# Performance work log

Measured on AMD Instinct MI355X. Metric: run time of the kernel, lower is better.

The kernel has to match this reference:

```python
import jax, jax.numpy as jnp
import numpy as np
from jax import lax

B, P, W, C = 32, 256, 16, 64
H = 128          # hidden_dim
PRED = 64        # pred_stat_len
TOK = W + 1      # token_len
SIGMA_MIN = 1e-3
EPS = 1e-5


def setup_inputs() -> dict:
    key = jax.random.key(0)
    ks = jax.random.split(key, 20)
    s = 0.05
    inp = {
        "mu_hist": jax.random.normal(ks[0], (B, P, C), jnp.float32),
        "std_hist": jax.random.uniform(ks[1], (B, P, C), jnp.float32, 0.1, 1.5),
        "anchor": jax.random.normal(ks[2], (B, 1, C), jnp.float32),
        "raw_patches": jax.random.normal(ks[3], (B, P, W, C), jnp.float32),
        # mean branch params
        "mean_in_W": jax.random.normal(ks[4], (TOK, H), jnp.float32) * s,
        "mean_in_b": jax.random.normal(ks[5], (H,), jnp.float32) * s,
        "mean_a_logit": jnp.full((H,), float(np.log(9.0)), jnp.float32),
        "mean_post_W": jax.random.normal(ks[6], (H, H), jnp.float32) * s,
        "mean_post_b": jax.random.normal(ks[7], (H,), jnp.float32) * s,
        "mean_out_W": jax.random.normal(ks[8], (H, PRED), jnp.float32) * s,
        "mean_out_b": jax.random.normal(ks[9], (PRED,), jnp.float32) * s,
        "gamma_mu": jax.random.normal(ks[10], (C,), jnp.float32) * s,
        # std branch params
        "std_in_W": jax.random.normal(ks[11], (TOK, H), jnp.float32) * s,
        "std_in_b": jax.random.normal(ks[12], (H,), jnp.float32) * s,
        "std_a_logit": jnp.full((H,), float(np.log(9.0)), jnp.float32),
        "std_post_W": jax.random.normal(ks[13], (H, H), jnp.float32) * s,
        "std_post_b": jax.random.normal(ks[14], (H,), jnp.float32) * s,
        "std_out_W": jax.random.normal(ks[15], (H, PRED), jnp.float32) * s,
        "std_out_b": jax.random.normal(ks[16], (PRED,), jnp.float32) * s,
        "gamma_std": jax.random.normal(ks[17], (C,), jnp.float32) * s,
    }
    return inp


def _ema(u, a_logit):
    # u: (BC, P, H) -> final hidden state (BC, H) via h_t = a*h + (1-a)*u_t
    a = jax.nn.sigmoid(a_logit)
    one_minus_a = 1.0 - a

    def step(h, u_t):
        return a * h + one_minus_a * u_t, None

    h0 = jnp.zeros((u.shape[0], u.shape[2]), u.dtype)
    h, _ = lax.scan(step, h0, jnp.swapaxes(u, 0, 1))  # scan over P
    return h


def _branch(token, in_W, in_b, a_logit, post_W, post_b, out_W, out_b):
    u = token @ in_W + in_b                     # (BC, P, H)
    h = _ema(u, a_logit)                        # (BC, H)
    h = h + jax.nn.gelu(h, approximate=False) @ post_W + post_b
    res = h @ out_W + out_b                     # (BC, PRED)
    return res.reshape(B, C, PRED).transpose(0, 2, 1)  # (B, PRED, C)


def reference(mu_hist, std_hist, anchor, raw_patches,
              mean_in_W, mean_in_b, mean_a_logit, mean_post_W, mean_post_b,
              mean_out_W, mean_out_b, gamma_mu,
              std_in_W, std_in_b, std_a_logit, std_post_W, std_post_b,
              std_out_W, std_out_b, gamma_std):
    BC = B * C
    # --- mean branch ---
    mu_center = mu_hist - anchor                                 # (B,P,C)
    raw_center = raw_patches - anchor[:, :, None, :]             # (B,P,W,C)
    mu_center_t = mu_center.transpose(0, 2, 1).reshape(BC, P, 1)
    raw_center_t = raw_center.transpose(0, 3, 1, 2).reshape(BC, P, W)
    mean_token = jnp.concatenate([mu_center_t, raw_center_t], axis=-1)
    mu_res = _branch(mean_token, mean_in_W, mean_in_b, mean_a_logit,
                     mean_post_W, mean_post_b, mean_out_W, mean_out_b)
    mu_fut = anchor + gamma_mu[None, None, :] * mu_res           # (B,PRED,C)

    # --- std branch ---
    logstd_hist = jnp.log(jnp.maximum(std_hist, SIGMA_MIN))      # (B,P,C)
    logstd_anchor = logstd_hist.mean(axis=1, keepdims=True)      # (B,1,C)
    logstd_center = logstd_hist - logstd_anchor
    z_patch = (raw_patches - mu_hist[:, :, None, :]) / (std_hist[:, :, None, :] + EPS)
    logstd_center_t = logstd_center.transpose(0, 2, 1).reshape(BC, P, 1)
    z_patch_t = z_patch.transpose(0, 3, 1, 2).reshape(BC, P, W)
    std_token = jnp.concatenate([logstd_center_t, z_patch_t], axis=-1)
    logstd_res = _branch(std_token, std_in_W, std_in_b, std_a_logit,
                         std_post_W, std_post_b, std_out_W, std_out_b)
    logstd_fut = logstd_anchor + gamma_std[None, None, :] * logstd_res
    std_fut = jnp.maximum(jnp.exp(logstd_fut), SIGMA_MIN)
    return mu_fut, std_fut
```

## Files before the change

kernel.cpp:

```cpp
#include <hip/hip_runtime.h>
#include <math.h>

#define Bn 32
#define Pn 256
#define Wn 16
#define Cn 64
#define Hn 128
#define PREDn 64
#define TOKn 17

__global__ void lsa_kernel(const float* __restrict__ std_hist,
                           float* __restrict__ lsa) {
  int b = blockIdx.x;
  int c = threadIdx.x & 63;
  int q = threadIdx.x >> 6;
  const float* base = std_hist + ((size_t)b * Pn) * Cn + c;
  float s = 0.f;
#pragma unroll
  for (int i = 0; i < 64; ++i) {
    int t = q + 4 * i;
    s += logf(fmaxf(base[(size_t)t * Cn], 1e-3f));
  }
  __shared__ float red[4][64];
  red[q][c] = s;
  __syncthreads();
  if (q == 0) {
    lsa[b * 64 + c] =
        (red[0][c] + red[1][c] + red[2][c] + red[3][c]) * (1.0f / 256.0f);
  }
}

__launch_bounds__(256, 2)
__global__ void ema_kernel(
    const float* __restrict__ mu_hist, const float* __restrict__ std_hist,
    const float* __restrict__ anchor, const float* __restrict__ raw,
    const float* __restrict__ mW, const float* __restrict__ mb, const float* __restrict__ mal,
    const float* __restrict__ sW, const float* __restrict__ sb, const float* __restrict__ sal,
    const float* __restrict__ lsa, float* __restrict__ Spart) {
  const int sx = blockIdx.x;
  const int cblk = sx & 1, hblk = (sx >> 1) & 1, ph = (sx >> 2) & 1;
  const int b = blockIdx.y, br = blockIdx.z;
  const int tid = threadIdx.x;
  const int cr = tid & 31;
  const int hhg = tid >> 5;

  const float* inW = br ? sW : mW;
  const float* inb = br ? sb : mb;
  const float* alog = br ? sal : mal;
  const int hh0 = hblk * 64 + hhg * 8;

  float Wr[TOKn][8];
#pragma unroll
  for (int k = 0; k < TOKn; ++k) {
    float4 w0 = *(const float4*)&inW[k * Hn + hh0];
    float4 w1 = *(const float4*)&inW[k * Hn + hh0 + 4];
    Wr[k][0] = w0.x; Wr[k][1] = w0.y; Wr[k][2] = w0.z; Wr[k][3] = w0.w;
    Wr[k][4] = w1.x; Wr[k][5] = w1.y; Wr[k][6] = w1.z; Wr[k][7] = w1.w;
  }
  float av[8], oma[8], bias[8], h[8];
#pragma unroll
  for (int i = 0; i < 8; ++i) {
    float a = 1.0f / (1.0f + expf(-alog[hh0 + i]));
    av[i] = a; oma[i] = 1.0f - a; bias[i] = inb[hh0 + i]; h[i] = 0.0f;
  }

  const int cs = cblk * 32 + cr;
  const size_t bP = (size_t)b * Pn;
  const float* rawb = raw + bP * Wn * Cn;
  const float* mub = mu_hist + bP * Cn;
  const float* stdb = std_hist + bP * Cn;
  const float anch_cs = anchor[b * Cn + cs];
  float anch2 = 0.f, lsa2 = 0.f;
  if (tid < 32) {
    anch2 = anchor[b * Cn + cblk * 32 + tid];
    lsa2 = lsa[b * Cn + cblk * 32 + tid];
  }

  __shared__ float tok[2][32][20];

  const int w0 = tid >> 5;
  const int t0 = ph * 128;

  auto stage = [&](int t, int buf) {
    const float* rawt = rawb + (size_t)t * (Wn * Cn);
    if (br == 0) {
      float r0 = rawt[w0 * Cn + cs];
      float r1 = rawt[(w0 + 8) * Cn + cs];
      tok[buf][cr][1 + w0] = r0 - anch_cs;
      tok[buf][cr][1 + w0 + 8] = r1 - anch_cs;
      if (tid < 32) {
        tok[buf][tid][0] = mub[(size_t)t * Cn + cblk * 32 + tid] - anch2;
      }
    } else {
      float mu = mub[(size_t)t * Cn + cs];
      float sd = stdb[(size_t)t * Cn + cs];
      float inv = 1.0f / (sd + 1e-5f);
      float r0 = rawt[w0 * Cn + cs];
      float r1 = rawt[(w0 + 8) * Cn + cs];
      tok[buf][cr][1 + w0] = (r0 - mu) * inv;
      tok[buf][cr][1 + w0 + 8] = (r1 - mu) * inv;
      if (tid < 32) {
        float sv = stdb[(size_t)t * Cn + cblk * 32 + tid];
        tok[buf][tid][0] = logf(fmaxf(sv, 1e-3f)) - lsa2;
      }
    }
  };

  stage(t0, 0);
  __syncthreads();
  int cur = 0;
  for (int tt = 0; tt < 128; ++tt) {
    if (tt + 1 < 128) stage(t0 + tt + 1, cur ^ 1);
    const float* row = &tok[cur][cr][0];
    float4 q0 = *(const float4*)(row);
    float4 q1 = *(const float4*)(row + 4);
    float4 q2 = *(const float4*)(row + 8);
    float4 q3 = *(const float4*)(row + 12);
    float q4 = row[16];
#pragma unroll
    for (int i = 0; i < 8; ++i) {
      float u = bias[i];
      u = fmaf(q0.x, Wr[0][i], u);
      u = fmaf(q0.y, Wr[1][i], u);
      u = fmaf(q0.z, Wr[2][i], u);
      u = fmaf(q0.w, Wr[3][i], u);
      u = fmaf(q1.x, Wr[4][i], u);
      u = fmaf(q1.y, Wr[5][i], u);
      u = fmaf(q1.z, Wr[6][i], u);
      u = fmaf(q1.w, Wr[7][i], u);
      u = fmaf(q2.x, Wr[8][i], u);
      u = fmaf(q2.y, Wr[9][i], u);
      u = fmaf(q2.z, Wr[10][i], u);
      u = fmaf(q2.w, Wr[11][i], u);
      u = fmaf(q3.x, Wr[12][i], u);
      u = fmaf(q3.y, Wr[13][i], u);
      u = fmaf(q3.z, Wr[14][i], u);
      u = fmaf(q3.w, Wr[15][i], u);
      u = fmaf(q4, Wr[16][i], u);
      h[i] = fmaf(av[i], h[i], oma[i] * u);
    }
    __syncthreads();
    cur ^= 1;
  }

  const int idx_block = (((br * 2 + ph) * Bn + b) * 2 + cblk) * 2 + hblk;
  float* op = Spart + (size_t)idx_block * 2048 + tid * 8;
  float4 o0 = {h[0], h[1], h[2], h[3]};
  float4 o1 = {h[4], h[5], h[6], h[7]};
  *(float4*)op = o0;
  *(float4*)(op + 4) = o1;
}

__launch_bounds__(128, 4)
__global__ void head_kernel(
    const float* __restrict__ anchor, const float* __restrict__ lsa,
    const float* __restrict__ mal, const float* __restrict__ mpW, const float* __restrict__ mpb,
    const float* __restrict__ moW, const float* __restrict__ mob, const float* __restrict__ gmu,
    const float* __restrict__ sal, const float* __restrict__ spW, const float* __restrict__ spb,
    const float* __restrict__ soW, const float* __restrict__ sob, const float* __restrict__ gst,
    const float* __restrict__ Spart, float* __restrict__ out) {
  const int br = blockIdx.y;
  const int bc0 = blockIdx.x * 8;
  const int tid = threadIdx.x;
  const float* alog = br ? sal : mal;
  const float* pW = br ? spW : mpW;
  const float* pb = br ? spb : mpb;
  const float* oW = br ? soW : moW;
  const float* ob = br ? sob : mob;

  __shared__ float smem[2048];
  float* g_lds = smem;
  float* h2 = smem + 1024;

  const float a = 1.0f / (1.0f + expf(-alog[tid]));
  float ap = a;
#pragma unroll
  for (int s7 = 0; s7 < 7; ++s7) ap *= ap;

  const int hblk = tid >> 6;
  const int hhg = (tid >> 3) & 7;
  const int ii = tid & 7;

  float hreg[8];
#pragma unroll
  for (int g = 0; g < 8; ++g) {
    int bc = bc0 + g;
    int bb = bc >> 6, cc = bc & 63;
    int cblk2 = cc >> 5, crr = cc & 31;
    size_t base0 = ((size_t)((((br * 2 + 0) * Bn + bb) * 2 + cblk2) * 2 + hblk)) * 2048 +
                   (hhg * 32 + crr) * 8 + ii;
    size_t base1 = ((size_t)((((br * 2 + 1) * Bn + bb) * 2 + cblk2) * 2 + hblk)) * 2048 +
                   (hhg * 32 + crr) * 8 + ii;
    float hv = fmaf(ap, Spart[base0], Spart[base1]);
    hreg[g] = hv;
    g_lds[g * 128 + tid] = 0.5f * hv * (1.0f + erff(hv * 0.70710678118654752f));
  }
  __syncthreads();

  float acc[8];
#pragma unroll
  for (int g = 0; g < 8; ++g) acc[g] = hreg[g] + pb[tid];
  for (int j = 0; j < 128; ++j) {
    float wv = pW[j * Hn + tid];
#pragma unroll
    for (int g = 0; g < 8; ++g) acc[g] = fmaf(g_lds[g * 128 + j], wv, acc[g]);
  }
#pragma unroll
  for (int g = 0; g < 8; ++g) h2[g * 128 + tid] = acc[g];
  __syncthreads();

  const int p = tid & 63;
  const int jh = tid >> 6;
  float s[8];
#pragma unroll
  for (int g = 0; g < 8; ++g) s[g] = 0.f;
  for (int j = jh * 64; j < jh * 64 + 64; ++j) {
    float wv = oW[j * PREDn + p];
#pragma unroll
    for (int g = 0; g < 8; ++g) s[g] = fmaf(h2[g * 128 + j], wv, s[g]);
  }
  float* red = smem;
#pragma unroll
  for (int g = 0; g < 8; ++g) red[jh * 512 + g * 64 + p] = s[g];
  __syncthreads();
  if (tid < 64) {
#pragma unroll
    for (int g = 0; g < 8; ++g) {
      int bc = bc0 + g;
      int bb = bc >> 6, cc = bc & 63;
      float tot = red[g * 64 + p] + red[512 + g * 64 + p] + ob[p];
      if (br == 0) {
        out[((size_t)bb * PREDn + p) * Cn + cc] = fmaf(gmu[cc], tot, anchor[bb * Cn + cc]);
      } else {
        float lf = fmaf(gst[cc], tot, lsa[bb * Cn + cc]);
        out[131072 + ((size_t)bb * PREDn + p) * Cn + cc] = fmaxf(expf(lf), 1e-3f);
      }
    }
  }
}

extern "C" void kernel_launch(void* const* d_in, const int* in_sizes, int n_in,
                              void* d_out, int out_size, void* d_ws, size_t ws_size,
                              hipStream_t stream) {
  (void)in_sizes; (void)n_in; (void)out_size; (void)ws_size;
  const float* mu_hist = (const float*)d_in[0];
  const float* std_hist = (const float*)d_in[1];
  const float* anchor = (const float*)d_in[2];
  const float* raw = (const float*)d_in[3];
  const float* mW = (const float*)d_in[4];
  const float* mb_ = (const float*)d_in[5];
  const float* mal = (const float*)d_in[6];
  const float* mpW = (const float*)d_in[7];
  const float* mpb = (const float*)d_in[8];
  const float* moW = (const float*)d_in[9];
  const float* mob = (const float*)d_in[10];
  const float* gmu = (const float*)d_in[11];
  const float* sW = (const float*)d_in[12];
  const float* sb_ = (const float*)d_in[13];
  const float* sal = (const float*)d_in[14];
  const float* spW = (const float*)d_in[15];
  const float* spb = (const float*)d_in[16];
  const float* soW = (const float*)d_in[17];
  const float* sob = (const float*)d_in[18];
  const float* gst = (const float*)d_in[19];
  float* out = (float*)d_out;
  float* ws = (float*)d_ws;

  float* lsa = ws;
  float* Spart = ws + 2048;

  hipLaunchKernelGGL(lsa_kernel, dim3(32), dim3(256), 0, stream, std_hist, lsa);
  hipLaunchKernelGGL(ema_kernel, dim3(8, 32, 2), dim3(256), 0, stream,
                     mu_hist, std_hist, anchor, raw, mW, mb_, mal, sW, sb_, sal, lsa, Spart);
  hipLaunchKernelGGL(head_kernel, dim3(256, 2), dim3(128), 0, stream,
                     anchor, lsa, mal, mpW, mpb, moW, mob, gmu,
                     sal, spW, spb, soW, sob, gst, Spart, out);
}
```

Before: 244.5 us.

## Move per-channel shifts out of EMA scan, batch timesteps per sync

The EMA kernel now stages four timesteps per barrier into a rotated, bank-conflict-avoiding shared layout, and loads from global one block ahead in registers. The anchor and log-std mean shifts are no longer subtracted per token. They are folded algebraically into the head kernel as a closed-form correction using the geometric decay and the summed input weights. This removes the dependency of the EMA kernel on lsa, so it could overlap with lsa_kernel. The head kernel's matvec loops are also vectorised with float4 LDS reads. The risks are small floating-point differences from applying the correction late, and higher register pressure from the buffered loads.

```diff
diff --git a/kernel.cpp b/kernel.cpp
--- a/kernel.cpp
+++ b/kernel.cpp
@@ -8,6 +8,8 @@
 #define Hn 128
 #define PREDn 64
 #define TOKn 17
+#define TBLK 4
+#define NPH 32
 
 __global__ void lsa_kernel(const float* __restrict__ std_hist,
                            float* __restrict__ lsa) {
@@ -33,35 +35,36 @@
 __launch_bounds__(256, 2)
 __global__ void ema_kernel(
     const float* __restrict__ mu_hist, const float* __restrict__ std_hist,
-    const float* __restrict__ anchor, const float* __restrict__ raw,
+    const float* __restrict__ raw,
     const float* __restrict__ mW, const float* __restrict__ mb, const float* __restrict__ mal,
     const float* __restrict__ sW, const float* __restrict__ sb, const float* __restrict__ sal,
-    const float* __restrict__ lsa, float* __restrict__ Spart) {
+    float* __restrict__ Spart) {
   const int sx = blockIdx.x;
   const int cblk = sx & 1, hblk = (sx >> 1) & 1, ph = (sx >> 2) & 1;
   const int b = blockIdx.y, br = blockIdx.z;
   const int tid = threadIdx.x;
   const int cr = tid & 31;
-  const int hhg = tid >> 5;
+  const int w0 = tid >> 5;
 
   const float* inW = br ? sW : mW;
   const float* inb = br ? sb : mb;
   const float* alog = br ? sal : mal;
-  const int hh0 = hblk * 64 + hhg * 8;
+  const int hh0 = hblk * 64 + w0 * 8;
 
   float Wr[TOKn][8];
 #pragma unroll
   for (int k = 0; k < TOKn; ++k) {
-    float4 w0 = *(const float4*)&inW[k * Hn + hh0];
-    float4 w1 = *(const float4*)&inW[k * Hn + hh0 + 4];
-    Wr[k][0] = w0.x; Wr[k][1] = w0.y; Wr[k][2] = w0.z; Wr[k][3] = w0.w;
-    Wr[k][4] = w1.x; Wr[k][5] = w1.y; Wr[k][6] = w1.z; Wr[k][7] = w1.w;
-  }
-  float av[8], oma[8], bias[8], h[8];
+    float4 wv0 = *(const float4*)&inW[k * Hn + hh0];
+    float4 wv1 = *(const float4*)&inW[k * Hn + hh0 + 4];
+    Wr[k][0] = wv0.x; Wr[k][1] = wv0.y; Wr[k][2] = wv0.z; Wr[k][3] = wv0.w;
+    Wr[k][4] = wv1.x; Wr[k][5] = wv1.y; Wr[k][6] = wv1.z; Wr[k][7] = wv1.w;
+  }
+  float av[8], bias[8], h[8];
 #pragma unroll
   for (int i = 0; i < 8; ++i) {
-    float a = 1.0f / (1.0f + expf(-alog[hh0 + i]));
-    av[i] = a; oma[i] = 1.0f - a; bias[i] = inb[hh0 + i]; h[i] = 0.0f;
+    av[i] = 1.0f / (1.0f + expf(-alog[hh0 + i]));
+    bias[i] = inb[hh0 + i];
+    h[i] = 0.0f;
   }
 
   const int cs = cblk * 32 + cr;
@@ -69,77 +72,112 @@
   const float* rawb = raw + bP * Wn * Cn;
   const float* mub = mu_hist + bP * Cn;
   const float* stdb = std_hist + bP * Cn;
-  const float anch_cs = anchor[b * Cn + cs];
-  float anch2 = 0.f, lsa2 = 0.f;
-  if (tid < 32) {
-    anch2 = anchor[b * Cn + cblk * 32 + tid];
-    lsa2 = lsa[b * Cn + cblk * 32 + tid];
-  }
-
-  __shared__ float tok[2][32][20];
-
-  const int w0 = tid >> 5;
+
+  __shared__ float tok[2][TBLK][32 * 20];
+
+  const int rot = (cr >> 3) & 3;
+  const int ro0 = cr * 20 + 4 * ((0 + rot) & 3);
+  const int ro1 = cr * 20 + 4 * ((1 + rot) & 3);
+  const int ro2 = cr * 20 + 4 * ((2 + rot) & 3);
+  const int ro3 = cr * 20 + 4 * ((3 + rot) & 3);
+  const int qo = cr * 20 + 16;
+
+  auto woff = [](int c, int f) {
+    if (f >= 16) return c * 20 + 16;
+    int r = (c >> 3) & 3;
+    return c * 20 + 4 * (((f >> 2) + r) & 3) + (f & 3);
+  };
+  const int f1 = 1 + w0, f2 = 9 + w0;
+  const int wf1 = woff(cr, f1);
+  const int wf2 = woff(cr, f2);
+  const int cmu = tid & 31;
+  const int tqmu = tid >> 5;
+  const int wf0 = woff(cmu, 0);
+  const int cmug = cblk * 32 + cmu;
+
   const int t0 = ph * 128;
 
-  auto stage = [&](int t, int buf) {
-    const float* rawt = rawb + (size_t)t * (Wn * Cn);
-    if (br == 0) {
-      float r0 = rawt[w0 * Cn + cs];
-      float r1 = rawt[(w0 + 8) * Cn + cs];
-      tok[buf][cr][1 + w0] = r0 - anch_cs;
-      tok[buf][cr][1 + w0 + 8] = r1 - anch_cs;
-      if (tid < 32) {
-        tok[buf][tid][0] = mub[(size_t)t * Cn + cblk * 32 + tid] - anch2;
+  float rA[TBLK], rB[TBLK], rC[TBLK], rD[TBLK], rM = 0.f;
+
+  auto LOAD = [&](int tb) {
+#pragma unroll
+    for (int tq = 0; tq < TBLK; ++tq) {
+      int t = tb + tq;
+      rA[tq] = rawb[(size_t)t * (Wn * Cn) + w0 * Cn + cs];
+      rB[tq] = rawb[(size_t)t * (Wn * Cn) + (w0 + 8) * Cn + cs];
+      if (br) {
+        rC[tq] = mub[(size_t)t * Cn + cs];
+        rD[tq] = stdb[(size_t)t * Cn + cs];
       }
-    } else {
-      float mu = mub[(size_t)t * Cn + cs];
-      float sd = stdb[(size_t)t * Cn + cs];
-      float inv = 1.0f / (sd + 1e-5f);
-      float r0 = rawt[w0 * Cn + cs];
-      float r1 = rawt[(w0 + 8) * Cn + cs];
-      tok[buf][cr][1 + w0] = (r0 - mu) * inv;
-      tok[buf][cr][1 + w0 + 8] = (r1 - mu) * inv;
-      if (tid < 32) {
-        float sv = stdb[(size_t)t * Cn + cblk * 32 + tid];
-        tok[buf][tid][0] = logf(fmaxf(sv, 1e-3f)) - lsa2;
+    }
+    if (tid < 128) {
+      int t = tb + tqmu;
+      rM = br ? stdb[(size_t)t * Cn + cmug] : mub[(size_t)t * Cn + cmug];
+    }
+  };
+
+  auto WRITE = [&](int buf) {
+#pragma unroll
+    for (int tq = 0; tq < TBLK; ++tq) {
+      if (br == 0) {
+        tok[buf][tq][wf1] = rA[tq];
+        tok[buf][tq][wf2] = rB[tq];
+      } else {
+        float inv = 1.0f / (rD[tq] + 1e-5f);
+        tok[buf][tq][wf1] = (rA[tq] - rC[tq]) * inv;
+        tok[buf][tq][wf2] = (rB[tq] - rC[tq]) * inv;
       }
     }
+    if (tid < 128) {
+      tok[buf][tqmu][wf0] = br ? logf(fmaxf(rM, 1e-3f)) : rM;
+    }
   };
 
-  stage(t0, 0);
+  auto COMPUTE = [&](int buf) {
+#pragma unroll
+    for (int tq = 0; tq < TBLK; ++tq) {
+      float4 q0 = *(const float4*)&tok[buf][tq][ro0];
+      float4 q1 = *(const float4*)&tok[buf][tq][ro1];
+      float4 q2 = *(const float4*)&tok[buf][tq][ro2];
+      float4 q3 = *(const float4*)&tok[buf][tq][ro3];
+      float q4 = tok[buf][tq][qo];
+#pragma unroll
+      for (int i = 0; i < 8; ++i) {
+        float u = bias[i];
+        u = fmaf(q0.x, Wr[0][i], u);
+        u = fmaf(q0.y, Wr[1][i], u);
+        u = fmaf(q0.z, Wr[2][i], u);
+        u = fmaf(q0.w, Wr[3][i], u);
+        u = fmaf(q1.x, Wr[4][i], u);
+        u = fmaf(q1.y, Wr[5][i], u);
+        u = fmaf(q1.z, Wr[6][i], u);
+        u = fmaf(q1.w, Wr[7][i], u);
+        u = fmaf(q2.x, Wr[8][i], u);
+        u = fmaf(q2.y, Wr[9][i], u);
+        u = fmaf(q2.z, Wr[10][i], u);
+        u = fmaf(q2.w, Wr[11][i], u);
+        u = fmaf(q3.x, Wr[12][i], u);
+        u = fmaf(q3.y, Wr[13][i], u);
+        u = fmaf(q3.z, Wr[14][i], u);
+        u = fmaf(q3.w, Wr[15][i], u);
+        u = fmaf(q4, Wr[16][i], u);
+        h[i] = fmaf(av[i], h[i] - u, u);
+      }
+    }
+  };
+
+  LOAD(t0);
+  WRITE(0);
   __syncthreads();
   int cur = 0;
-  for (int tt = 0; tt < 128; ++tt) {
-    if (tt + 1 < 128) stage(t0 + tt + 1, cur ^ 1);
-    const float* row = &tok[cur][cr][0];
-    float4 q0 = *(const float4*)(row);
-    float4 q1 = *(const float4*)(row + 4);
-    float4 q2 = *(const float4*)(row + 8);
-    float4 q3 = *(const float4*)(row + 12);
-    float q4 = row[16];
-#pragma unroll
-    for (int i = 0; i < 8; ++i) {
-      float u = bias[i];
-      u = fmaf(q0.x, Wr[0][i], u);
-      u = fmaf(q0.y, Wr[1][i], u);
-      u = fmaf(q0.z, Wr[2][i], u);
-      u = fmaf(q0.w, Wr[3][i], u);
-      u = fmaf(q1.x, Wr[4][i], u);
-      u = fmaf(q1.y, Wr[5][i], u);
-      u = fmaf(q1.z, Wr[6][i], u);
-      u = fmaf(q1.w, Wr[7][i], u);
-      u = fmaf(q2.x, Wr[8][i], u);
-      u = fmaf(q2.y, Wr[9][i], u);
-      u = fmaf(q2.z, Wr[10][i], u);
-      u = fmaf(q2.w, Wr[11][i], u);
-      u = fmaf(q3.x, Wr[12][i], u);
-      u = fmaf(q3.y, Wr[13][i], u);
-      u = fmaf(q3.z, Wr[14][i], u);
-      u = fmaf(q3.w, Wr[15][i], u);
-      u = fmaf(q4, Wr[16][i], u);
-      h[i] = fmaf(av[i], h[i], oma[i] * u);
-    }
-    __syncthreads();
+#pragma unroll 1
+  for (int p = 0; p < NPH; ++p) {
+    if (p + 1 < NPH) LOAD(t0 + (p + 1) * TBLK);
+    COMPUTE(cur);
+    if (p + 1 < NPH) {
+      WRITE(cur ^ 1);
+      __syncthreads();
+    }
     cur ^= 1;
   }
 
@@ -154,6 +192,7 @@
 __launch_bounds__(128, 4)
 __global__ void head_kernel(
     const float* __restrict__ anchor, const float* __restrict__ lsa,
+    const float* __restrict__ mW, const float* __restrict__ sW,
     const float* __restrict__ mal, const float* __restrict__ mpW, const float* __restrict__ mpb,
     const float* __restrict__ moW, const float* __restrict__ mob, const float* __restrict__ gmu,
     const float* __restrict__ sal, const float* __restrict__ spW, const float* __restrict__ spb,
@@ -176,6 +215,17 @@
   float ap = a;
 #pragma unroll
   for (int s7 = 0; s7 < 7; ++s7) ap *= ap;
+  const float apF = ap * ap;
+  float SWv;
+  if (br == 0) {
+    float s = 0.f;
+#pragma unroll
+    for (int k = 0; k < TOKn; ++k) s += mW[k * Hn + tid];
+    SWv = s;
+  } else {
+    SWv = sW[tid];
+  }
+  const float cS = (1.0f - apF) * SWv;
 
   const int hblk = tid >> 6;
   const int hhg = (tid >> 3) & 7;
@@ -191,7 +241,9 @@
                    (hhg * 32 + crr) * 8 + ii;
     size_t base1 = ((size_t)((((br * 2 + 1) * Bn + bb) * 2 + cblk2) * 2 + hblk)) * 2048 +
                    (hhg * 32 + crr) * 8 + ii;
+    float shiftv = br ? lsa[bb * Cn + cc] : anchor[bb * Cn + cc];
     float hv = fmaf(ap, Spart[base0], Spart[base1]);
+    hv = fmaf(-cS, shiftv, hv);
     hreg[g] = hv;
     g_lds[g * 128 + tid] = 0.5f * hv * (1.0f + erff(hv * 0.70710678118654752f));
   }
@@ -200,10 +252,19 @@
   float acc[8];
 #pragma unroll
   for (int g = 0; g < 8; ++g) acc[g] = hreg[g] + pb[tid];
-  for (int j = 0; j < 128; ++j) {
-    float wv = pW[j * Hn + tid];
-#pragma unroll
-    for (int g = 0; g < 8; ++g) acc[g] = fmaf(g_lds[g * 128 + j], wv, acc[g]);
+  for (int j = 0; j < 128; j += 4) {
+    float w0v = pW[j * Hn + tid];
+    float w1v = pW[(j + 1) * Hn + tid];
+    float w2v = pW[(j + 2) * Hn + tid];
+    float w3v = pW[(j + 3) * Hn + tid];
+#pragma unroll
+    for (int g = 0; g < 8; ++g) {
+      float4 gv = *(const float4*)&g_lds[g * 128 + j];
+      acc[g] = fmaf(gv.x, w0v, acc[g]);
+      acc[g] = fmaf(gv.y, w1v, acc[g]);
+      acc[g] = fmaf(gv.z, w2v, acc[g]);
+      acc[g] = fmaf(gv.w, w3v, acc[g]);
+    }
   }
 #pragma unroll
   for (int g = 0; g < 8; ++g) h2[g * 128 + tid] = acc[g];
@@ -214,10 +275,20 @@
   float s[8];
 #pragma unroll
   for (int g = 0; g < 8; ++g) s[g] = 0.f;
-  for (int j = jh * 64; j < jh * 64 + 64; ++j) {
-    float wv = oW[j * PREDn + p];
-#pragma unroll
-    for (int g = 0; g < 8; ++g) s[g] = fmaf(h2[g * 128 + j], wv, s[g]);
+  for (int jj = 0; jj < 64; jj += 4) {
+    int j = jh * 64 + jj;
+    float w0v = oW[j * PREDn + p];
+    float w1v = oW[(j + 1) * PREDn + p];
+    float w2v = oW[(j + 2) * PREDn + p];
+    float w3v = oW[(j + 3) * PREDn + p];
+#pragma unroll
+    for (int g = 0; g < 8; ++g) {
+      float4 hv4 = *(const float4*)&h2[g * 128 + j];
+      s[g] = fmaf(hv4.x, w0v, s[g]);
+      s[g] = fmaf(hv4.y, w1v, s[g]);
+      s[g] = fmaf(hv4.z, w2v, s[g]);
+      s[g] = fmaf(hv4.w, w3v, s[g]);
+    }
   }
   float* red = smem;
 #pragma unroll
@@ -271,8 +342,8 @@
 
   hipLaunchKernelGGL(lsa_kernel, dim3(32), dim3(256), 0, stream, std_hist, lsa);
   hipLaunchKernelGGL(ema_kernel, dim3(8, 32, 2), dim3(256), 0, stream,
-                     mu_hist, std_hist, anchor, raw, mW, mb_, mal, sW, sb_, sal, lsa, Spart);
+                     mu_hist, std_hist, raw, mW, mb_, mal, sW, sb_, sal, Spart);
   hipLaunchKernelGGL(head_kernel, dim3(256, 2), dim3(128), 0, stream,
-                     anchor, lsa, mal, mpW, mpb, moW, mob, gmu,
+                     anchor, lsa, mW, sW, mal, mpW, mpb, moW, mob, gmu,
                      sal, spW, spb, soW, sob, gst, Spart, out);
 }
```

Result: slower. 284.6 us (+16.4%).
